# Kernel tuning notes

Measured on AMD Instinct MI355X. Metric: run time of the kernel, lower is better.

## Reference

```python
import jax, jax.numpy as jnp
import numpy as np

SEQ, B, D, T = 512, 128, 1024, 32  # seq_len, batch, input_dim, num_tags


def setup_inputs() -> dict:
    key = jax.random.key(0)
    ks = jax.random.split(key, 6)
    return {
        "features": jax.random.normal(ks[0], (SEQ, B, D), jnp.float32),
        "mask": jnp.ones((SEQ, B), jnp.int32),
        "W": jax.random.normal(ks[1], (T, D), jnp.float32) * 0.02,   # features_to_tag weight
        "b": jnp.zeros((T,), jnp.float32),                            # features_to_tag bias
        "transition": jax.random.normal(ks[2], (T, T), jnp.float32) * 0.1,
        "start_probs": jax.random.normal(ks[3], (T,), jnp.float32) * 0.1,
        "end_probs": jax.random.normal(ks[4], (T,), jnp.float32) * 0.1,
    }


def _alpha(emissions, maskf, trans, start):
    # forward recursion: alpha[i, b, j] = logsumexp_k(alpha[i-1,b,k] + trans[k,j]) + e[i,b,j]
    a0 = emissions[0] + start[None, :]
    def step(prev, xs):
        e, m = xs
        new = jax.nn.logsumexp(prev[:, :, None] + trans[None] + e[:, None, :], axis=1)
        nxt = m[:, None] * new + (1.0 - m)[:, None] * prev
        return nxt, nxt
    _, rest = jax.lax.scan(step, a0, (emissions[1:], maskf[1:]))
    return jnp.concatenate([a0[None], rest], axis=0)  # (S,B,T)


def _beta(emissions, maskf, trans, end):
    # backward recursion: beta[i-1, b, j] = logsumexp_k(beta[i,b,k] + e[i,b,k] + trans[j,k])
    bL = jnp.broadcast_to(end[None, :], emissions.shape[1:])  # (B,T)
    def step(prev, xs):
        e, m = xs
        s = prev + e  # (B,T)
        new = jax.nn.logsumexp(s[:, None, :] + trans[None], axis=2)
        nxt = m[:, None] * new + (1.0 - m)[:, None] * prev
        return nxt, nxt
    _, rest = jax.lax.scan(step, bL, (emissions[1:], maskf[1:]), reverse=True)
    return jnp.concatenate([rest, bL[None]], axis=0)  # (S,B,T)


def _viterbi(emissions, mask, trans, start, end):
    s0 = start[None, :] + emissions[0]  # (B,T)
    def step(score, xs):
        e, m = xs
        cand = score[:, :, None] + trans[None] + e[:, None, :]  # (B,T_from,T_to)
        nxt = jnp.max(cand, axis=1)
        idx = jnp.argmax(cand, axis=1).astype(jnp.int32)
        score = jnp.where(m[:, None].astype(bool), nxt, score)
        return score, idx
    score, history = jax.lax.scan(step, s0, (emissions[1:], mask[1:]))
    score = score + end[None, :]
    last = jnp.argmax(score, axis=1).astype(jnp.int32)  # (B,)
    def back(tag, hist):
        new = jnp.take_along_axis(hist, tag[:, None], axis=1)[:, 0]
        return new, new
    _, tags_rest = jax.lax.scan(back, last, history, reverse=True)
    return jnp.concatenate([tags_rest, last[None]], axis=0)  # (S,B)


def reference(features, mask, W, b, transition, start_probs, end_probs):
    emissions = jnp.einsum("sbd,td->sbt", features, W) + b  # (S,B,T)
    maskf = mask.astype(emissions.dtype)
    alpha = _alpha(emissions, maskf, transition, start_probs)
    beta = _beta(emissions, maskf, transition, end_probs)
    z = jax.nn.logsumexp(alpha[-1] + end_probs[None, :], axis=1)  # (B,)
    probs = jnp.exp(alpha + beta - z[None, :, None])  # marginal probabilities
    tags = _viterbi(emissions, mask, transition, start_probs, end_probs)
    return probs, tags
```

## Files before the change

kernel.cpp:

```cpp
#include <hip/hip_runtime.h>

#define SEQ 512
#define BATCH 128
#define DIM 1024
#define T 32

__device__ __forceinline__ float rlf(float x, int n) {
    return __int_as_float(__builtin_amdgcn_readlane(__float_as_int(x), n));
}

__device__ __forceinline__ int mbit(unsigned long long m0, unsigned long long m1,
        unsigned long long m2, unsigned long long m3, unsigned long long m4,
        unsigned long long m5, unsigned long long m6, unsigned long long m7, int i) {
    int w = i >> 6;
    unsigned long long cm =
        (w < 4) ? ((w < 2) ? (w == 0 ? m0 : m1) : (w == 2 ? m2 : m3))
                : ((w < 6) ? (w == 4 ? m4 : m5) : (w == 6 ? m6 : m7));
    return (int)((cm >> (i & 63)) & 1ULL);
}

#define BALLOTS(pre, bb) \
    unsigned long long pre##0 = __ballot(mask[(0 * 64 + tid) * BATCH + (bb)] != 0); \
    unsigned long long pre##1 = __ballot(mask[(1 * 64 + tid) * BATCH + (bb)] != 0); \
    unsigned long long pre##2 = __ballot(mask[(2 * 64 + tid) * BATCH + (bb)] != 0); \
    unsigned long long pre##3 = __ballot(mask[(3 * 64 + tid) * BATCH + (bb)] != 0); \
    unsigned long long pre##4 = __ballot(mask[(4 * 64 + tid) * BATCH + (bb)] != 0); \
    unsigned long long pre##5 = __ballot(mask[(5 * 64 + tid) * BATCH + (bb)] != 0); \
    unsigned long long pre##6 = __ballot(mask[(6 * 64 + tid) * BATCH + (bb)] != 0); \
    unsigned long long pre##7 = __ballot(mask[(7 * 64 + tid) * BATCH + (bb)] != 0);

#define MB(pre, i) mbit(pre##0, pre##1, pre##2, pre##3, pre##4, pre##5, pre##6, pre##7, (i))

#define MATVEC32(dst, src, Et) { \
    float q0 = 0.f, q1 = 0.f, q2 = 0.f, q3 = 0.f; \
    _Pragma("unroll") \
    for (int n = 0; n < 8; ++n) { \
        q0 = fmaf(rlf(src, 4 * n + 0), Et[4 * n + 0], q0); \
        q1 = fmaf(rlf(src, 4 * n + 1), Et[4 * n + 1], q1); \
        q2 = fmaf(rlf(src, 4 * n + 2), Et[4 * n + 2], q2); \
        q3 = fmaf(rlf(src, 4 * n + 3), Et[4 * n + 3], q3); \
    } \
    dst = (q0 + q1) + (q2 + q3); }

#define RLSUM32(dst, src) { \
    float s0 = 0.f, s1 = 0.f, s2 = 0.f, s3 = 0.f; \
    _Pragma("unroll") \
    for (int n = 0; n < 8; ++n) { \
        s0 += rlf(src, 4 * n + 0); \
        s1 += rlf(src, 4 * n + 1); \
        s2 += rlf(src, 4 * n + 2); \
        s3 += rlf(src, 4 * n + 3); \
    } \
    dst = (s0 + s1) + (s2 + s3); }

#define STAGE(blk) do { \
    _Pragma("unroll") \
    for (int ps = 0; ps < 16; ++ps) { \
        int r = ps * 8 + r8; \
        float4 v = *(const float4*)&e[(size_t)(((blk) * 128 + r) * BATCH + b) * T + q * 4]; \
        *(float4*)&ebuf[(blk) & 1][r * 32 + q * 4] = v; \
    } } while (0)

#define FLUSHPC(dstP, dstC, blk) do { \
    _Pragma("unroll") \
    for (int ps = 0; ps < 16; ++ps) { \
        int r = ps * 8 + r8; \
        float4 v = *(const float4*)&pbuf[(blk) & 1][r * 32 + q * 4]; \
        *(float4*)&dstP[(size_t)(((blk) * 128 + r) * BATCH + b) * T + q * 4] = v; \
    } \
    _Pragma("unroll") \
    for (int ps = 0; ps < 2; ++ps) { \
        int r = ps * 64 + tid; \
        dstC[(size_t)((blk) * 128 + r) * BATCH + b] = cbuf[(blk) & 1][r]; \
    } } while (0)

__global__ void k_wt(const float* __restrict__ W, float* __restrict__ Wt)
{
    int idx = blockIdx.x * 256 + threadIdx.x;
    if (idx >= DIM * T) return;
    int d = idx >> 5, t = idx & 31;
    Wt[idx] = W[t * DIM + d];
}

__global__ __launch_bounds__(256) void k_emis(const float* __restrict__ A,
        const float* __restrict__ Wt, const float* __restrict__ bias,
        float* __restrict__ e)
{
    __shared__ float lds[64 * 37];
    int tid = threadIdx.x;
    int row0 = blockIdx.x * 64;
    int row = tid & 63;
    int grp = __builtin_amdgcn_readfirstlane(tid >> 6);
    int q = tid & 7;
    int rb = tid >> 3;

    float acc[8];
    #pragma unroll
    for (int t = 0; t < 8; ++t) acc[t] = bias[grp * 8 + t];

    const float* A0 = &A[(size_t)(row0 + rb) * DIM];
    const float* A1 = &A[(size_t)(row0 + rb + 32) * DIM];

    float4 v0 = *(const float4*)&A0[q * 4];
    float4 v1 = *(const float4*)&A1[q * 4];

    for (int ck = 0; ck < 32; ++ck) {
        lds[rb * 37 + q * 4 + 0] = v0.x;
        lds[rb * 37 + q * 4 + 1] = v0.y;
        lds[rb * 37 + q * 4 + 2] = v0.z;
        lds[rb * 37 + q * 4 + 3] = v0.w;
        lds[(rb + 32) * 37 + q * 4 + 0] = v1.x;
        lds[(rb + 32) * 37 + q * 4 + 1] = v1.y;
        lds[(rb + 32) * 37 + q * 4 + 2] = v1.z;
        lds[(rb + 32) * 37 + q * 4 + 3] = v1.w;
        __syncthreads();
        if (ck < 31) {
            v0 = *(const float4*)&A0[(ck + 1) * 32 + q * 4];
            v1 = *(const float4*)&A1[(ck + 1) * 32 + q * 4];
        }
        #pragma unroll
        for (int d = 0; d < 32; ++d) {
            float av = lds[row * 37 + d];
            const float* wrow = &Wt[(ck * 32 + d) * T + grp * 8];
            #pragma unroll
            for (int t = 0; t < 8; ++t)
                acc[t] = fmaf(av, wrow[t], acc[t]);
        }
        __syncthreads();
    }

    float4* eo = (float4*)&e[(size_t)(row0 + row) * T + grp * 8];
    float4 o0, o1;
    o0.x = acc[0]; o0.y = acc[1]; o0.z = acc[2]; o0.w = acc[3];
    o1.x = acc[4]; o1.y = acc[5]; o1.z = acc[6]; o1.w = acc[7];
    eo[0] = o0; eo[1] = o1;
}

__global__ __launch_bounds__(64) void k_rec(const float* __restrict__ e,
        const int* __restrict__ mask,
        const float* __restrict__ trans,
        const float* __restrict__ start,
        const float* __restrict__ endp,
        float* __restrict__ pa, float* __restrict__ pb,
        double* __restrict__ Ca, double* __restrict__ Cb,
        double* __restrict__ zd,
        float* __restrict__ tags_out)
{
    __shared__ float  ebuf[2][128 * 32];
    __shared__ float  pbuf[2][128 * 32];
    __shared__ double cbuf[2][128];
    __shared__ int    tagbuf[SEQ];

    int bid = blockIdx.x;
    int tid = threadIdx.x;
    int j   = tid & 31;
    int role = bid >> 7;
    int b    = bid & 127;
    int r8 = tid >> 3, q = tid & 7;

    BALLOTS(ma, b);

    if (role == 0) {
        float Et[32];
        #pragma unroll
        for (int n = 0; n < 32; ++n) Et[n] = __expf(trans[n * T + j]);

        STAGE(0);
        float a0 = ebuf[0][j] + start[j];
        float m = a0;
        #pragma unroll
        for (int d = 1; d < 32; d <<= 1) m = fmaxf(m, __shfl_xor(m, d));
        float v = __expf(a0 - m);
        float s = v;
        #pragma unroll
        for (int d = 1; d < 32; d <<= 1) s += __shfl_xor(s, d);
        float p = v / s;
        double C = (double)m + (double)__logf(s);
        if (tid < 32) pbuf[0][j] = p;
        if (tid == 0) cbuf[0][0] = C;

        for (int c = 0; c < 4; ++c) {
            int i0 = c ? c * 128 : 1, i1 = c * 128 + 127;
            for (int i = i0; i <= i1; ++i) {
                float eraw = ebuf[c & 1][(i & 127) * 32 + j];
                float q_;
                MATVEC32(q_, p, Et);
                float ee = __expf(eraw);
                float vv = q_ * ee;
                if (MB(ma, i)) p = vv;
                if (tid < 32) pbuf[c & 1][(i & 127) * 32 + j] = p;
                if (tid == 0) cbuf[c & 1][i & 127] = C;
                if ((i & 7) == 0) {
                    float ss; RLSUM32(ss, p);
                    p = p / ss; C += (double)__logf(ss);
                }
            }
            if (c < 3) STAGE(c + 1);
            FLUSHPC(pa, Ca, c);
        }
        float sz0 = p * __expf(endp[j]);
        float sz; RLSUM32(sz, sz0);
        if (tid == 0) zd[b] = C + (double)__logf(sz);
    } else if (role == 1) {
        float Et[32];
        #pragma unroll
        for (int n = 0; n < 32; ++n) Et[n] = __expf(trans[j * T + n]);

        STAGE(3);
        float v0 = endp[j];
        float m = v0;
        #pragma unroll
        for (int d = 1; d < 32; d <<= 1) m = fmaxf(m, __shfl_xor(m, d));
        float v = __expf(v0 - m);
        float s = v;
        #pragma unroll
        for (int d = 1; d < 32; d <<= 1) s += __shfl_xor(s, d);
        float p = v / s;
        double C = (double)m + (double)__logf(s);
        if (tid < 32) pbuf[1][127 * 32 + j] = p;
        if (tid == 0) cbuf[1][127] = C;

        float eraw = ebuf[1][127 * 32 + j];
        for (int c = 0; c < 4; ++c) {
            int iS = 511 - 128 * c;
            int iE = (c < 3) ? (384 - 128 * c) : 1;
            for (int i = iS; i >= iE; --i) {
                float ee = __expf(eraw);
                if (i > iE)
                    eraw = ebuf[((i - 1) >> 7) & 1][((i - 1) & 127) * 32 + j];
                float pe = p * ee;
                float q_;
                MATVEC32(q_, pe, Et);
                if (MB(ma, i)) p = q_;
                int orow = i - 1, lb = (orow >> 7) & 1;
                if (tid < 32) pbuf[lb][(orow & 127) * 32 + j] = p;
                if (tid == 0) cbuf[lb][orow & 127] = C;
                if ((i & 7) == 0) {
                    float ss; RLSUM32(ss, p);
                    p = p / ss; C += (double)__logf(ss);
                }
            }
            if (c < 3) {
                STAGE(2 - c);
                eraw = ebuf[(2 - c) & 1][127 * 32 + j];
            }
            FLUSHPC(pb, Cb, 3 - c);
        }
    } else {
        unsigned char* hist = (unsigned char*)pbuf;

        float trv[32];
        #pragma unroll
        for (int n = 0; n < 32; ++n) trv[n] = trans[n * T + j];

        STAGE(0);
        float sc = start[j] + ebuf[0][j];

        for (int c = 0; c < 4; ++c) {
            int i0 = c ? c * 128 : 1, i1 = c * 128 + 127;
            for (int i = i0; i <= i1; ++i) {
                float ej = ebuf[c & 1][(i & 127) * 32 + j];
                float c_[32];
                #pragma unroll
                for (int n = 0; n < 32; ++n)
                    c_[n] = (rlf(sc, n) + trv[n]) + ej;
                float v1[16]; int i1_[16];
                #pragma unroll
                for (int n = 0; n < 16; ++n) {
                    bool t = c_[2 * n] >= c_[2 * n + 1];
                    v1[n] = t ? c_[2 * n] : c_[2 * n + 1];
                    i1_[n] = t ? 2 * n : 2 * n + 1;
                }
                float v2[8]; int i2[8];
                #pragma unroll
                for (int n = 0; n < 8; ++n) {
                    bool t = v1[2 * n] >= v1[2 * n + 1];
                    v2[n] = t ? v1[2 * n] : v1[2 * n + 1];
                    i2[n] = t ? i1_[2 * n] : i1_[2 * n + 1];
                }
                float v3[4]; int i3[4];
                #pragma unroll
                for (int n = 0; n < 4; ++n) {
                    bool t = v2[2 * n] >= v2[2 * n + 1];
                    v3[n] = t ? v2[2 * n] : v2[2 * n + 1];
                    i3[n] = t ? i2[2 * n] : i2[2 * n + 1];
                }
                float v4[2]; int i4[2];
                #pragma unroll
                for (int n = 0; n < 2; ++n) {
                    bool t = v3[2 * n] >= v3[2 * n + 1];
                    v4[n] = t ? v3[2 * n] : v3[2 * n + 1];
                    i4[n] = t ? i3[2 * n] : i3[2 * n + 1];
                }
                bool t = v4[0] >= v4[1];
                float best = t ? v4[0] : v4[1];
                int bi = t ? i4[0] : i4[1];

                if (tid < 32) hist[(i - 1) * T + j] = (unsigned char)bi;
                if (MB(ma, i)) sc = best;
            }
            if (c < 3) STAGE(c + 1);
        }
        float fs = sc + endp[j];
        int fj = j;
        #pragma unroll
        for (int d = 1; d < 32; d <<= 1) {
            float ov = __shfl_xor(fs, d);
            int oj = __shfl_xor(fj, d);
            if (ov > fs || (ov == fs && oj < fj)) { fs = ov; fj = oj; }
        }
        if (tid == 0) {
            int tag = fj;
            tagbuf[SEQ - 1] = tag;
            for (int i = SEQ - 2; i >= 0; --i) {
                tag = hist[i * T + tag];
                tagbuf[i] = tag;
            }
        }
        __syncthreads();
        #pragma unroll
        for (int k2 = 0; k2 < 8; ++k2) {
            int idx = k2 * 64 + tid;
            tags_out[(size_t)idx * BATCH + b] = (float)tagbuf[idx];
        }
    }
}

__global__ __launch_bounds__(256) void k_probs(const float* __restrict__ pa,
        const float* __restrict__ pb, const double* __restrict__ Ca,
        const double* __restrict__ Cb, const double* __restrict__ zd,
        float* __restrict__ out)
{
    int idx = blockIdx.x * 256 + threadIdx.x;
    int ib = idx >> 3;
    int b = ib & (BATCH - 1);
    double ex = Ca[ib] + Cb[ib] - zd[b];
    double scl = exp(ex);
    float4 a = ((const float4*)pa)[idx];
    float4 c = ((const float4*)pb)[idx];
    float4 o;
    o.x = (float)((double)a.x * (double)c.x * scl);
    o.y = (float)((double)a.y * (double)c.y * scl);
    o.z = (float)((double)a.z * (double)c.z * scl);
    o.w = (float)((double)a.w * (double)c.w * scl);
    ((float4*)out)[idx] = o;
}

extern "C" void kernel_launch(void* const* d_in, const int* in_sizes, int n_in,
                              void* d_out, int out_size, void* d_ws, size_t ws_size,
                              hipStream_t stream) {
    const float* features = (const float*)d_in[0];
    const int*   mask     = (const int*)d_in[1];
    const float* W        = (const float*)d_in[2];
    const float* bias     = (const float*)d_in[3];
    const float* trans    = (const float*)d_in[4];
    const float* startp   = (const float*)d_in[5];
    const float* endp     = (const float*)d_in[6];

    char* ws = (char*)d_ws;
    double* Ca = (double*)(ws + 0);
    double* Cb = (double*)(ws + 524288);
    double* zd = (double*)(ws + 1048576);
    float*  Wt = (float*)(ws + 1049600);
    float*  e  = (float*)(ws + 1180672);
    float*  pa = (float*)(ws + 9569280);
    float*  pb = (float*)(ws + 17957888);

    float* probs_out = (float*)d_out;
    float* tags_out  = probs_out + (size_t)SEQ * BATCH * T;

    k_wt<<<128, 256, 0, stream>>>(W, Wt);
    k_emis<<<1024, 256, 0, stream>>>(features, Wt, bias, e);
    k_rec<<<384, 64, 0, stream>>>(e, mask, trans, startp, endp,
                                  pa, pb, Ca, Cb, zd, tags_out);
    k_probs<<<2048, 256, 0, stream>>>(pa, pb, Ca, Cb, zd, probs_out);
}
```

Measured before the change: 349.1 us.

## Interleave two batches per Viterbi wave, vectorize backtrace, pre-exp emissions at staging

The Viterbi blocks now each handle two batch rows, interleaving two independent max-plus recurrences to hide latency, and the grid shrinks from 384 to 320 blocks. The serial single-lane backtrace is replaced by a readlane-based walk over history chunks held in registers. The forward and backward roles exponentiate emissions once while staging them into shared memory, which removes the expf from the serial loop. In exchange, Viterbi blocks do twice the work per step, which may lengthen the critical path if the interleaving does not overlap well.

```diff
diff --git a/kernel.cpp b/kernel.cpp
--- a/kernel.cpp
+++ b/kernel.cpp
@@ -53,11 +53,12 @@
     } \
     dst = (s0 + s1) + (s2 + s3); }
 
-#define STAGE(blk) do { \
+#define STAGEXP(blk) do { \
     _Pragma("unroll") \
     for (int ps = 0; ps < 16; ++ps) { \
         int r = ps * 8 + r8; \
         float4 v = *(const float4*)&e[(size_t)(((blk) * 128 + r) * BATCH + b) * T + q * 4]; \
+        v.x = __expf(v.x); v.y = __expf(v.y); v.z = __expf(v.z); v.w = __expf(v.w); \
         *(float4*)&ebuf[(blk) & 1][r * 32 + q * 4] = v; \
     } } while (0)
 
@@ -73,6 +74,51 @@
         int r = ps * 64 + tid; \
         dstC[(size_t)((blk) * 128 + r) * BATCH + b] = cbuf[(blk) & 1][r]; \
     } } while (0)
+
+#define STAGEV(blk) do { \
+    _Pragma("unroll") \
+    for (int ps = 0; ps < 8; ++ps) { \
+        int r = ps * 8 + r8; \
+        float4 vA = *(const float4*)&e[(size_t)(((blk) * 64 + r) * BATCH + bA) * T + q * 4]; \
+        float4 vB = *(const float4*)&e[(size_t)(((blk) * 64 + r) * BATCH + bB) * T + q * 4]; \
+        *(float4*)&eA[(blk) & 1][r * 32 + q * 4] = vA; \
+        *(float4*)&eB[(blk) & 1][r * 32 + q * 4] = vB; \
+    } } while (0)
+
+#define VITSTEP(best, bi, sc, ej) { \
+    float c_[32]; \
+    _Pragma("unroll") \
+    for (int n = 0; n < 32; ++n) c_[n] = (rlf(sc, n) + trv[n]) + (ej); \
+    float w1[16]; int x1[16]; \
+    _Pragma("unroll") \
+    for (int n = 0; n < 16; ++n) { bool t = c_[2*n] >= c_[2*n+1]; w1[n] = t ? c_[2*n] : c_[2*n+1]; x1[n] = t ? 2*n : 2*n+1; } \
+    float w2[8]; int x2[8]; \
+    _Pragma("unroll") \
+    for (int n = 0; n < 8; ++n) { bool t = w1[2*n] >= w1[2*n+1]; w2[n] = t ? w1[2*n] : w1[2*n+1]; x2[n] = t ? x1[2*n] : x1[2*n+1]; } \
+    float w3[4]; int x3[4]; \
+    _Pragma("unroll") \
+    for (int n = 0; n < 4; ++n) { bool t = w2[2*n] >= w2[2*n+1]; w3[n] = t ? w2[2*n] : w2[2*n+1]; x3[n] = t ? x2[2*n] : x2[2*n+1]; } \
+    float w4[2]; int x4[2]; \
+    _Pragma("unroll") \
+    for (int n = 0; n < 2; ++n) { bool t = w3[2*n] >= w3[2*n+1]; w4[n] = t ? w3[2*n] : w3[2*n+1]; x4[n] = t ? x3[2*n] : x3[2*n+1]; } \
+    bool tt = w4[0] >= w4[1]; \
+    best = tt ? w4[0] : w4[1]; \
+    bi = tt ? x4[0] : x4[1]; }
+
+#define BACKTRACE(hist, tgbuf, fj_) { \
+    int tag = __builtin_amdgcn_readfirstlane(fj_); \
+    _Pragma("unroll 1") \
+    for (int g = 31; g >= 0; --g) { \
+        int h[16]; \
+        _Pragma("unroll") \
+        for (int k = 0; k < 16; ++k) h[k] = hist[(16 * g + k) * 32 + j]; \
+        if (g == 31) h[15] = j;    \
+        _Pragma("unroll") \
+        for (int k = 15; k >= 0; --k) { \
+            tag = __builtin_amdgcn_readlane(h[k], tag); \
+            tgbuf[16 * g + k] = (unsigned char)tag; \
+        } \
+    } }
 
 __global__ void k_wt(const float* __restrict__ W, float* __restrict__ Wt)
 {
@@ -146,182 +192,159 @@
         double* __restrict__ zd,
         float* __restrict__ tags_out)
 {
-    __shared__ float  ebuf[2][128 * 32];
-    __shared__ float  pbuf[2][128 * 32];
-    __shared__ double cbuf[2][128];
-    __shared__ int    tagbuf[SEQ];
-
+    __shared__ __align__(16) char smem[67584];
     int bid = blockIdx.x;
     int tid = threadIdx.x;
     int j   = tid & 31;
-    int role = bid >> 7;
-    int b    = bid & 127;
     int r8 = tid >> 3, q = tid & 7;
 
-    BALLOTS(ma, b);
-
-    if (role == 0) {
+    if (bid < 256) {
+        int role = bid >> 7;
+        int b    = bid & 127;
+        float (*ebuf)[4096] = (float(*)[4096])smem;
+        float (*pbuf)[4096] = (float(*)[4096])(smem + 32768);
+        double (*cbuf)[128] = (double(*)[128])(smem + 65536);
+
+        BALLOTS(ma, b);
         float Et[32];
-        #pragma unroll
-        for (int n = 0; n < 32; ++n) Et[n] = __expf(trans[n * T + j]);
-
-        STAGE(0);
-        float a0 = ebuf[0][j] + start[j];
-        float m = a0;
-        #pragma unroll
-        for (int d = 1; d < 32; d <<= 1) m = fmaxf(m, __shfl_xor(m, d));
-        float v = __expf(a0 - m);
-        float s = v;
-        #pragma unroll
-        for (int d = 1; d < 32; d <<= 1) s += __shfl_xor(s, d);
-        float p = v / s;
-        double C = (double)m + (double)__logf(s);
-        if (tid < 32) pbuf[0][j] = p;
-        if (tid == 0) cbuf[0][0] = C;
-
-        for (int c = 0; c < 4; ++c) {
-            int i0 = c ? c * 128 : 1, i1 = c * 128 + 127;
-            for (int i = i0; i <= i1; ++i) {
-                float eraw = ebuf[c & 1][(i & 127) * 32 + j];
-                float q_;
-                MATVEC32(q_, p, Et);
-                float ee = __expf(eraw);
-                float vv = q_ * ee;
-                if (MB(ma, i)) p = vv;
-                if (tid < 32) pbuf[c & 1][(i & 127) * 32 + j] = p;
-                if (tid == 0) cbuf[c & 1][i & 127] = C;
-                if ((i & 7) == 0) {
-                    float ss; RLSUM32(ss, p);
-                    p = p / ss; C += (double)__logf(ss);
+
+        if (role == 0) {
+            #pragma unroll
+            for (int n = 0; n < 32; ++n) Et[n] = __expf(trans[n * T + j]);
+
+            STAGEXP(0);
+            float a0 = e[(0 * BATCH + b) * T + j] + start[j];
+            float m = a0;
+            #pragma unroll
+            for (int d = 1; d < 32; d <<= 1) m = fmaxf(m, __shfl_xor(m, d));
+            float v = __expf(a0 - m);
+            float s = v;
+            #pragma unroll
+            for (int d = 1; d < 32; d <<= 1) s += __shfl_xor(s, d);
+            float p = v / s;
+            double C = (double)m + (double)__logf(s);
+            if (tid < 32) pbuf[0][j] = p;
+            if (tid == 0) cbuf[0][0] = C;
+
+            for (int c = 0; c < 4; ++c) {
+                int i0 = c ? c * 128 : 1, i1 = c * 128 + 127;
+                for (int i = i0; i <= i1; ++i) {
+                    float ee = ebuf[c & 1][(i & 127) * 32 + j];
+                    float q_;
+                    MATVEC32(q_, p, Et);
+                    float vv = q_ * ee;
+                    if (MB(ma, i)) p = vv;
+                    if (tid < 32) pbuf[c & 1][(i & 127) * 32 + j] = p;
+                    if (tid == 0) cbuf[c & 1][i & 127] = C;
+                    if ((i & 7) == 0) {
+                        float ss; RLSUM32(ss, p);
+                        p = p / ss; C += (double)__logf(ss);
+                    }
                 }
+                if (c < 3) STAGEXP(c + 1);
+                FLUSHPC(pa, Ca, c);
             }
-            if (c < 3) STAGE(c + 1);
-            FLUSHPC(pa, Ca, c);
-        }
-        float sz0 = p * __expf(endp[j]);
-        float sz; RLSUM32(sz, sz0);
-        if (tid == 0) zd[b] = C + (double)__logf(sz);
-    } else if (role == 1) {
-        float Et[32];
-        #pragma unroll
-        for (int n = 0; n < 32; ++n) Et[n] = __expf(trans[j * T + n]);
-
-        STAGE(3);
-        float v0 = endp[j];
-        float m = v0;
-        #pragma unroll
-        for (int d = 1; d < 32; d <<= 1) m = fmaxf(m, __shfl_xor(m, d));
-        float v = __expf(v0 - m);
-        float s = v;
-        #pragma unroll
-        for (int d = 1; d < 32; d <<= 1) s += __shfl_xor(s, d);
-        float p = v / s;
-        double C = (double)m + (double)__logf(s);
-        if (tid < 32) pbuf[1][127 * 32 + j] = p;
-        if (tid == 0) cbuf[1][127] = C;
-
-        float eraw = ebuf[1][127 * 32 + j];
-        for (int c = 0; c < 4; ++c) {
-            int iS = 511 - 128 * c;
-            int iE = (c < 3) ? (384 - 128 * c) : 1;
-            for (int i = iS; i >= iE; --i) {
-                float ee = __expf(eraw);
-                if (i > iE)
-                    eraw = ebuf[((i - 1) >> 7) & 1][((i - 1) & 127) * 32 + j];
-                float pe = p * ee;
-                float q_;
-                MATVEC32(q_, pe, Et);
-                if (MB(ma, i)) p = q_;
-                int orow = i - 1, lb = (orow >> 7) & 1;
-                if (tid < 32) pbuf[lb][(orow & 127) * 32 + j] = p;
-                if (tid == 0) cbuf[lb][orow & 127] = C;
-                if ((i & 7) == 0) {
-                    float ss; RLSUM32(ss, p);
-                    p = p / ss; C += (double)__logf(ss);
+            float sz0 = p * __expf(endp[j]);
+            float sz; RLSUM32(sz, sz0);
+            if (tid == 0) zd[b] = C + (double)__logf(sz);
+        } else {
+            #pragma unroll
+            for (int n = 0; n < 32; ++n) Et[n] = __expf(trans[j * T + n]);
+
+            STAGEXP(3);
+            float v0 = endp[j];
+            float m = v0;
+            #pragma unroll
+            for (int d = 1; d < 32; d <<= 1) m = fmaxf(m, __shfl_xor(m, d));
+            float v = __expf(v0 - m);
+            float s = v;
+            #pragma unroll
+            for (int d = 1; d < 32; d <<= 1) s += __shfl_xor(s, d);
+            float p = v / s;
+            double C = (double)m + (double)__logf(s);
+            if (tid < 32) pbuf[1][127 * 32 + j] = p;
+            if (tid == 0) cbuf[1][127] = C;
+
+            float een = ebuf[1][127 * 32 + j];
+            for (int c = 0; c < 4; ++c) {
+                int iS = 511 - 128 * c;
+                int iE = (c < 3) ? (384 - 128 * c) : 1;
+                for (int i = iS; i >= iE; --i) {
+                    float ee = een;
+                    if (i > iE)
+                        een = ebuf[((i - 1) >> 7) & 1][((i - 1) & 127) * 32 + j];
+                    float pe = p * ee;
+                    float q_;
+                    MATVEC32(q_, pe, Et);
+                    if (MB(ma, i)) p = q_;
+                    int orow = i - 1, lb = (orow >> 7) & 1;
+                    if (tid < 32) pbuf[lb][(orow & 127) * 32 + j] = p;
+                    if (tid == 0) cbuf[lb][orow & 127] = C;
+                    if ((i & 7) == 0) {
+                        float ss; RLSUM32(ss, p);
+                        p = p / ss; C += (double)__logf(ss);
+                    }
                 }
+                if (c < 3) {
+                    STAGEXP(2 - c);
+                    een = ebuf[(2 - c) & 1][127 * 32 + j];
+                }
+                FLUSHPC(pb, Cb, 3 - c);
             }
-            if (c < 3) {
-                STAGE(2 - c);
-                eraw = ebuf[(2 - c) & 1][127 * 32 + j];
-            }
-            FLUSHPC(pb, Cb, 3 - c);
         }
     } else {
-        unsigned char* hist = (unsigned char*)pbuf;
+        int bA = (bid - 256) * 2, bB = bA + 1;
+        float (*eA)[2048] = (float(*)[2048])smem;
+        float (*eB)[2048] = (float(*)[2048])(smem + 16384);
+        unsigned char* hA  = (unsigned char*)(smem + 32768);
+        unsigned char* hB  = (unsigned char*)(smem + 49152);
+        unsigned char* tgA = (unsigned char*)(smem + 65536);
+        unsigned char* tgB = tgA + 512;
+
+        BALLOTS(ma, bA);
+        BALLOTS(mb, bB);
 
         float trv[32];
         #pragma unroll
         for (int n = 0; n < 32; ++n) trv[n] = trans[n * T + j];
 
-        STAGE(0);
-        float sc = start[j] + ebuf[0][j];
-
-        for (int c = 0; c < 4; ++c) {
-            int i0 = c ? c * 128 : 1, i1 = c * 128 + 127;
+        STAGEV(0);
+        float scA = start[j] + eA[0][j];
+        float scB = start[j] + eB[0][j];
+
+        for (int c = 0; c < 8; ++c) {
+            int i0 = c ? c * 64 : 1, i1 = c * 64 + 63;
             for (int i = i0; i <= i1; ++i) {
-                float ej = ebuf[c & 1][(i & 127) * 32 + j];
-                float c_[32];
-                #pragma unroll
-                for (int n = 0; n < 32; ++n)
-                    c_[n] = (rlf(sc, n) + trv[n]) + ej;
-                float v1[16]; int i1_[16];
-                #pragma unroll
-                for (int n = 0; n < 16; ++n) {
-                    bool t = c_[2 * n] >= c_[2 * n + 1];
-                    v1[n] = t ? c_[2 * n] : c_[2 * n + 1];
-                    i1_[n] = t ? 2 * n : 2 * n + 1;
+                float ejA = eA[c & 1][(i & 63) * 32 + j];
+                float ejB = eB[c & 1][(i & 63) * 32 + j];
+                float bestA, bestB; int biA, biB;
+                VITSTEP(bestA, biA, scA, ejA);
+                VITSTEP(bestB, biB, scB, ejB);
+                if (tid < 32) {
+                    hA[(i - 1) * 32 + j] = (unsigned char)biA;
+                    hB[(i - 1) * 32 + j] = (unsigned char)biB;
                 }
-                float v2[8]; int i2[8];
-                #pragma unroll
-                for (int n = 0; n < 8; ++n) {
-                    bool t = v1[2 * n] >= v1[2 * n + 1];
-                    v2[n] = t ? v1[2 * n] : v1[2 * n + 1];
-                    i2[n] = t ? i1_[2 * n] : i1_[2 * n + 1];
-                }
-                float v3[4]; int i3[4];
-                #pragma unroll
-                for (int n = 0; n < 4; ++n) {
-                    bool t = v2[2 * n] >= v2[2 * n + 1];
-                    v3[n] = t ? v2[2 * n] : v2[2 * n + 1];
-                    i3[n] = t ? i2[2 * n] : i2[2 * n + 1];
-                }
-                float v4[2]; int i4[2];
-                #pragma unroll
-                for (int n = 0; n < 2; ++n) {
-                    bool t = v3[2 * n] >= v3[2 * n + 1];
-                    v4[n] = t ? v3[2 * n] : v3[2 * n + 1];
-                    i4[n] = t ? i3[2 * n] : i3[2 * n + 1];
-                }
-                bool t = v4[0] >= v4[1];
-                float best = t ? v4[0] : v4[1];
-                int bi = t ? i4[0] : i4[1];
-
-                if (tid < 32) hist[(i - 1) * T + j] = (unsigned char)bi;
-                if (MB(ma, i)) sc = best;
+                if (MB(ma, i)) scA = bestA;
+                if (MB(mb, i)) scB = bestB;
             }
-            if (c < 3) STAGE(c + 1);
-        }
-        float fs = sc + endp[j];
-        int fj = j;
+            if (c < 7) STAGEV(c + 1);
+        }
+        float fsA = scA + endp[j]; int fjA = j;
+        float fsB = scB + endp[j]; int fjB = j;
         #pragma unroll
         for (int d = 1; d < 32; d <<= 1) {
-            float ov = __shfl_xor(fs, d);
-            int oj = __shfl_xor(fj, d);
-            if (ov > fs || (ov == fs && oj < fj)) { fs = ov; fj = oj; }
-        }
-        if (tid == 0) {
-            int tag = fj;
-            tagbuf[SEQ - 1] = tag;
-            for (int i = SEQ - 2; i >= 0; --i) {
-                tag = hist[i * T + tag];
-                tagbuf[i] = tag;
-            }
-        }
-        __syncthreads();
+            float ovA = __shfl_xor(fsA, d); int ojA = __shfl_xor(fjA, d);
+            if (ovA > fsA || (ovA == fsA && ojA < fjA)) { fsA = ovA; fjA = ojA; }
+            float ovB = __shfl_xor(fsB, d); int ojB = __shfl_xor(fjB, d);
+            if (ovB > fsB || (ovB == fsB && ojB < fjB)) { fsB = ovB; fjB = ojB; }
+        }
+        BACKTRACE(hA, tgA, fjA);
+        BACKTRACE(hB, tgB, fjB);
         #pragma unroll
         for (int k2 = 0; k2 < 8; ++k2) {
             int idx = k2 * 64 + tid;
-            tags_out[(size_t)idx * BATCH + b] = (float)tagbuf[idx];
+            tags_out[(size_t)idx * BATCH + bA] = (float)tgA[idx];
+            tags_out[(size_t)idx * BATCH + bB] = (float)tgB[idx];
         }
     }
 }
@@ -371,7 +394,7 @@
 
     k_wt<<<128, 256, 0, stream>>>(W, Wt);
     k_emis<<<1024, 256, 0, stream>>>(features, Wt, bias, e);
-    k_rec<<<384, 64, 0, stream>>>(e, mask, trans, startp, endp,
+    k_rec<<<320, 64, 0, stream>>>(e, mask, trans, startp, endp,
                                   pa, pb, Ca, Cb, zd, tags_out);
     k_probs<<<2048, 256, 0, stream>>>(pa, pb, Ca, Cb, zd, probs_out);
 }
```

Result: slower. 664.4 us (+90.3%).
